# Kernel optimization log

Hardware: AMD Instinct MI355X
Metric: run time of the kernel (lower is better)

Reference implementation:

```python
import jax, jax.numpy as jnp
import numpy as np

N = 100_000   # num nodes
E = 1_600_000 # num directed edges (avg degree 16)
F_IN = 128    # num_features
HID = 128     # hidden_channels
C = 64        # num_classes
BN_EPS = 1e-5


def setup_inputs() -> dict:
    key = jax.random.key(0)
    ks = jax.random.split(key, 12)
    x = jax.random.normal(ks[0], (N, F_IN), dtype=jnp.float32)
    edge_index = jax.random.randint(ks[1], (2, E), 0, N, dtype=jnp.int32)
    def lin(k, fi, fo):
        s = 1.0 / np.sqrt(fi)
        return jax.random.uniform(k, (fi, fo), jnp.float32, -s, s)
    W1 = lin(ks[2], F_IN, HID)
    b1 = jnp.zeros((HID,), jnp.float32)
    W2 = lin(ks[3], HID, HID)
    b2 = jnp.zeros((HID,), jnp.float32)
    Wout = lin(ks[4], F_IN + 2 * HID, C)  # skip concat: 128 + 2*128 = 384
    bout = jnp.zeros((C,), jnp.float32)
    gamma = jnp.ones((HID,), jnp.float32)   # shared BatchNorm1d weight
    beta = jnp.zeros((HID,), jnp.float32)
    return {"x": x, "edge_index": edge_index, "W1": W1, "b1": b1,
            "W2": W2, "b2": b2, "Wout": Wout, "bout": bout,
            "gamma": gamma, "beta": beta}


def _gcn_norm(edge_index, n):
    # add self loops, then symmetric normalization (PyG GCNConv default)
    src, dst = edge_index[0], edge_index[1]
    loop = jnp.arange(n, dtype=src.dtype)
    src = jnp.concatenate([src, loop])
    dst = jnp.concatenate([dst, loop])
    deg = jax.ops.segment_sum(jnp.ones(src.shape[0], jnp.float32), dst, num_segments=n)
    dinv = jnp.where(deg > 0, jax.lax.rsqrt(deg), 0.0)
    norm = dinv[src] * dinv[dst]  # [E+N]
    return src, dst, norm


def _gcn_conv(h, src, dst, norm, n, W, b):
    h = h @ W                         # [n, out]
    msg = h[src] * norm[:, None]      # gather + scale, [E+n, out]
    return jax.ops.segment_sum(msg, dst, num_segments=n) + b


def _batchnorm(h, gamma, beta):
    # BatchNorm1d in training mode: biased batch statistics over nodes
    m = jnp.mean(h, axis=0)
    v = jnp.mean((h - m) ** 2, axis=0)
    return gamma * (h - m) * jax.lax.rsqrt(v + BN_EPS) + beta


def reference(x, edge_index, W1, b1, W2, b2, Wout, bout, gamma, beta):
    n = x.shape[0]
    src, dst, norm = _gcn_norm(edge_index, n)
    h1 = _batchnorm(jax.nn.relu(_gcn_conv(x, src, dst, norm, n, W1, b1)), gamma, beta)
    h2 = _batchnorm(jax.nn.relu(_gcn_conv(h1, src, dst, norm, n, W2, b2)), gamma, beta)
    hcat = jnp.concatenate([x, h1, h2], axis=1)  # skip concat [n, 384]
    return jax.nn.relu(_gcn_conv(hcat, src, dst, norm, n, Wout, bout))
```

## Files before the change

### kernel.cpp

```cpp
#include <hip/hip_runtime.h>
#include <cstdint>
#include <cstddef>

#define BN_EPS 1e-5f
#define NBLK 256
#define EPBMAX 6400
#define BCAP 4096
#define NBANK 32

typedef __attribute__((ext_vector_type(8))) short  bf16x8;
typedef __attribute__((ext_vector_type(4))) float  f32x4;
typedef __attribute__((ext_vector_type(8))) unsigned short ushort8;

__device__ __forceinline__ float bf2f(unsigned short u) {
  union { unsigned int i; float f; } c; c.i = ((unsigned int)u) << 16; return c.f;
}
__device__ __forceinline__ unsigned short f2bf(float f) {
  union { float f; unsigned int i; } c; c.f = f;
  unsigned int u = c.i;
  return (unsigned short)((u + 0x7FFFu + ((u >> 16) & 1u)) >> 16);
}

__global__ __launch_bounds__(256) void k_part(const int* __restrict__ src, const int* __restrict__ dst, int e, int epb,
                                              int* __restrict__ pairsG, int* __restrict__ cntT, int* __restrict__ scanT) {
  __shared__ int sbuf[EPBMAX];
  __shared__ int hist[1024];
  __shared__ int base[1024];
  __shared__ int tmp[256];
  int tid = threadIdx.x, b = blockIdx.x;
  int e0 = b * epb, e1 = min(e0 + epb, e);
  for (int i = tid; i < 1024; i += 256) hist[i] = 0;
  __syncthreads();
  for (int i = e0 + tid; i < e1; i += 256) atomicAdd(&hist[dst[i] >> 7], 1);
  __syncthreads();
  int c0 = hist[tid * 4], c1 = hist[tid * 4 + 1], c2 = hist[tid * 4 + 2], c3 = hist[tid * 4 + 3];
  int lsum = c0 + c1 + c2 + c3;
  tmp[tid] = lsum; __syncthreads();
  for (int off = 1; off < 256; off <<= 1) {
    int t = (tid >= off) ? tmp[tid - off] : 0; __syncthreads();
    tmp[tid] += t; __syncthreads();
  }
  int excl = tmp[tid] - lsum;
  base[tid * 4] = excl; base[tid * 4 + 1] = excl + c0;
  base[tid * 4 + 2] = excl + c0 + c1; base[tid * 4 + 3] = excl + c0 + c1 + c2;
  *(int4*)(cntT + b * 1024 + tid * 4) = make_int4(c0, c1, c2, c3);
  *(int4*)(scanT + b * 1024 + tid * 4) = make_int4(base[tid * 4], base[tid * 4 + 1], base[tid * 4 + 2], base[tid * 4 + 3]);
  __syncthreads();
  for (int i = e0 + tid; i < e1; i += 256) {
    int d = dst[i], s = src[i];
    int p = atomicAdd(&base[d >> 7], 1);
    sbuf[p] = ((d & 127) << 25) | s;
  }
  __syncthreads();
  int cnt = e1 - e0;
  for (int i = tid; i < cnt; i += 256) pairsG[e0 + i] = sbuf[i];
}

__global__ __launch_bounds__(256) void k_btot(const int* __restrict__ cntT, int* __restrict__ totals) {
  int k = blockIdx.x, tid = threadIdx.x;
  __shared__ int tmp[256];
  tmp[tid] = cntT[tid * 1024 + k];
  __syncthreads();
  for (int s = 128; s > 0; s >>= 1) {
    if (tid < s) tmp[tid] += tmp[tid + s];
    __syncthreads();
  }
  if (tid == 0) totals[k] = tmp[0];
}

__global__ __launch_bounds__(1024) void k_bscan(const int* __restrict__ totals, int* __restrict__ bbase, int nb, int e) {
  __shared__ int tmp[1024];
  int tid = threadIdx.x;
  int v = (tid < nb) ? totals[tid] : 0;
  tmp[tid] = v; __syncthreads();
  for (int off = 1; off < 1024; off <<= 1) {
    int t = (tid >= off) ? tmp[tid - off] : 0; __syncthreads();
    tmp[tid] += t; __syncthreads();
  }
  if (tid < nb) bbase[tid] = tmp[tid] - v;
  if (tid == 0) bbase[nb] = e;
}

__global__ __launch_bounds__(256) void k_build(const int* __restrict__ pairsG, const int* __restrict__ cntT,
                                               const int* __restrict__ scanT, const int* __restrict__ bbase_,
                                               int epb, int n, int nb,
                                               int* __restrict__ rowptr, int* __restrict__ colG, float* __restrict__ dinvG) {
  __shared__ int lpair[BCAP];
  __shared__ int lcol[BCAP];
  __shared__ int lcnt[128], lcur[128];
  __shared__ int tmp[256];
  int k = blockIdx.x, tid = threadIdx.x;
  int len = cntT[tid * 1024 + k];
  int sbase = tid * epb + scanT[tid * 1024 + k];
  tmp[tid] = len; __syncthreads();
  for (int off = 1; off < 256; off <<= 1) {
    int t = (tid >= off) ? tmp[tid - off] : 0; __syncthreads();
    tmp[tid] += t; __syncthreads();
  }
  int dpos = tmp[tid] - len;
  int cnt = tmp[255];
  for (int i = 0; i < len; ++i) lpair[dpos + i] = pairsG[sbase + i];
  if (tid < 128) lcnt[tid] = 0;
  __syncthreads();
  for (int j = tid; j < cnt; j += 256) atomicAdd(&lcnt[((unsigned)lpair[j]) >> 25], 1);
  __syncthreads();
  if (tid < 128) tmp[tid] = lcnt[tid];
  __syncthreads();
  for (int off = 1; off < 128; off <<= 1) {
    int t = (tid >= off && tid < 128) ? tmp[tid - off] : 0; __syncthreads();
    if (tid < 128) tmp[tid] += t;
    __syncthreads();
  }
  int bb = bbase_[k];
  if (tid < 128) {
    int excl = tmp[tid] - lcnt[tid];
    lcur[tid] = excl;
    int g = k * 128 + tid;
    if (g < n) {
      rowptr[g] = bb + excl;
      dinvG[g] = rsqrtf((float)lcnt[tid] + 1.0f);
    }
  }
  if (k == nb - 1 && tid == 0) rowptr[n] = bb + cnt;
  __syncthreads();
  for (int j = tid; j < cnt; j += 256) {
    int w = lpair[j];
    int p = atomicAdd(&lcur[((unsigned)w) >> 25], 1);
    lcol[p] = w & 0x01FFFFFF;
  }
  __syncthreads();
  for (int j = tid; j < cnt; j += 256) colG[bb + j] = lcol[j];
}

__global__ __launch_bounds__(256) void k_cvtw(const float* __restrict__ W1, const float* __restrict__ W2,
                                              const float* __restrict__ W3,
                                              unsigned short* __restrict__ Wt1, unsigned short* __restrict__ Wt2,
                                              unsigned short* __restrict__ Wt3) {
  int b = blockIdx.x, t = threadIdx.x;
  if (b < 64) {
    int idx = b * 256 + t; int k = idx >> 7, c = idx & 127;
    Wt1[c * 128 + k] = f2bf(W1[idx]);
  } else if (b < 128) {
    int idx = (b - 64) * 256 + t; int k = idx >> 7, c = idx & 127;
    Wt2[c * 128 + k] = f2bf(W2[idx]);
  } else {
    int idx = (b - 128) * 256 + t; int k = idx >> 6, c = idx & 63;
    Wt3[c * 384 + k] = f2bf(W3[idx]);
  }
}

template <int MODE>
__global__ __launch_bounds__(256) void k_gemm128(const void* __restrict__ Ap, const unsigned short* __restrict__ Bt,
                                                 const float* __restrict__ ss, const float* __restrict__ dinv,
                                                 unsigned short* __restrict__ C, int n) {
  __shared__ unsigned short As[128 * 128];
  __shared__ unsigned short Bs[128 * 128];
  __shared__ float ssl[256];
  const int tid = threadIdx.x;
  const int row0 = blockIdx.x * 128;
  if (MODE == 1 && tid < 256) ssl[tid] = ss[tid];

  {
    int colr = tid >> 1;
    int cbase = (tid & 1) * 8;
#pragma unroll
    for (int i = 0; i < 8; ++i) {
      int c16 = (cbase + i) * 16;
      int dstb = colr * 256 + (c16 ^ ((colr & 7) << 4));
      ushort8 v = *reinterpret_cast<const ushort8*>(Bt + colr * 128 + (c16 >> 1));
      *reinterpret_cast<ushort8*>((char*)Bs + dstb) = v;
    }
  }
  if (MODE == 1) __syncthreads();
  {
    int r = tid >> 1;
    int gr = row0 + r;
    int cbase = (tid & 1) * 8;
#pragma unroll
    for (int i = 0; i < 8; ++i) {
      int c16 = (cbase + i) * 16;
      int dstb = r * 256 + (c16 ^ ((r & 7) << 4));
      int f0 = c16 >> 1;
      ushort8 v = (ushort8)0;
      if (gr < n) {
        if (MODE == 0) {
          const float* A = (const float*)Ap;
          f32x4 v0 = *reinterpret_cast<const f32x4*>(A + (size_t)gr * 128 + f0);
          f32x4 v1 = *reinterpret_cast<const f32x4*>(A + (size_t)gr * 128 + f0 + 4);
#pragma unroll
          for (int j = 0; j < 4; ++j) { v[j] = f2bf(v0[j]); v[4 + j] = f2bf(v1[j]); }
        } else {
          const unsigned short* A = (const unsigned short*)Ap;
          ushort8 raw = *reinterpret_cast<const ushort8*>(A + (size_t)gr * 128 + f0);
#pragma unroll
          for (int j = 0; j < 8; ++j) v[j] = f2bf(bf2f(raw[j]) * ssl[f0 + j] + ssl[128 + f0 + j]);
        }
      }
      *reinterpret_cast<ushort8*>((char*)As + dstb) = v;
    }
  }
  __syncthreads();

  const int wv = tid >> 6;
  const int l = tid & 63;
  const int lr = l & 15;
  const int lk = l >> 4;

  f32x4 acc[2][8];
#pragma unroll
  for (int mi = 0; mi < 2; ++mi)
#pragma unroll
    for (int ni = 0; ni < 8; ++ni) acc[mi][ni] = (f32x4)0.f;

#pragma unroll
  for (int kt = 0; kt < 4; ++kt) {
    int kbyte = kt * 64 + lk * 16;
    bf16x8 aF[2], bF[8];
#pragma unroll
    for (int mi = 0; mi < 2; ++mi) {
      int r = wv * 32 + mi * 16 + lr;
      aF[mi] = *reinterpret_cast<bf16x8*>((char*)As + r * 256 + (kbyte ^ ((r & 7) << 4)));
    }
#pragma unroll
    for (int ni = 0; ni < 8; ++ni) {
      int c = ni * 16 + lr;
      bF[ni] = *reinterpret_cast<bf16x8*>((char*)Bs + c * 256 + (kbyte ^ ((c & 7) << 4)));
    }
#pragma unroll
    for (int mi = 0; mi < 2; ++mi)
#pragma unroll
      for (int ni = 0; ni < 8; ++ni)
        acc[mi][ni] = __builtin_amdgcn_mfma_f32_16x16x32_bf16(aF[mi], bF[ni], acc[mi][ni], 0, 0, 0);
  }

#pragma unroll
  for (int mi = 0; mi < 2; ++mi) {
#pragma unroll
    for (int i = 0; i < 4; ++i) {
      int gr = row0 + wv * 32 + mi * 16 + lk * 4 + i;
      if (gr < n) {
        float di = dinv[gr];
#pragma unroll
        for (int ni = 0; ni < 8; ++ni) {
          int gc = ni * 16 + lr;
          C[(size_t)gr * 128 + gc] = f2bf(acc[mi][ni][i] * di);
        }
      }
    }
  }
}

__global__ __launch_bounds__(256) void k_gemm3(const float* __restrict__ x, const unsigned short* __restrict__ a1,
                                               const unsigned short* __restrict__ a2,
                                               const float* __restrict__ ss1, const float* __restrict__ ss2,
                                               const unsigned short* __restrict__ Bt3, const float* __restrict__ dinv,
                                               unsigned short* __restrict__ C, int n) {
  __shared__ unsigned short As[128 * 128];
  __shared__ unsigned short Bs[64 * 384];
  __shared__ float ssl[512];
  const int tid = threadIdx.x;
  const int row0 = blockIdx.x * 128;
  if (tid < 256) { ssl[tid] = ss1[tid]; ssl[256 + tid] = ss2[tid]; }

  {
    int colr = tid >> 2;
    int cb = tid & 3;
#pragma unroll
    for (int i = 0; i < 12; ++i) {
      int c16 = (cb + 4 * i) * 16;
      int dstb = colr * 768 + (c16 ^ ((colr & 7) << 4));
      ushort8 v = *reinterpret_cast<const ushort8*>(Bt3 + colr * 384 + (c16 >> 1));
      *reinterpret_cast<ushort8*>((char*)Bs + dstb) = v;
    }
  }

  const int wv = tid >> 6;
  const int l = tid & 63;
  const int lr = l & 15;
  const int lk = l >> 4;

  f32x4 acc[2][4];
#pragma unroll
  for (int mi = 0; mi < 2; ++mi)
#pragma unroll
    for (int ni = 0; ni < 4; ++ni) acc[mi][ni] = (f32x4)0.f;

  for (int ch = 0; ch < 3; ++ch) {
    __syncthreads();
    {
      int r = tid >> 1;
      int gr = row0 + r;
      int cbase = (tid & 1) * 8;
#pragma unroll
      for (int i = 0; i < 8; ++i) {
        int c16 = (cbase + i) * 16;
        int dstb = r * 256 + (c16 ^ ((r & 7) << 4));
        int f0 = c16 >> 1;
        ushort8 v = (ushort8)0;
        if (gr < n) {
          if (ch == 0) {
            f32x4 v0 = *reinterpret_cast<const f32x4*>(x + (size_t)gr * 128 + f0);
            f32x4 v1 = *reinterpret_cast<const f32x4*>(x + (size_t)gr * 128 + f0 + 4);
#pragma unroll
            for (int j = 0; j < 4; ++j) { v[j] = f2bf(v0[j]); v[4 + j] = f2bf(v1[j]); }
          } else {
            const unsigned short* A = (ch == 1) ? a1 : a2;
            const float* sl = ssl + (ch - 1) * 256;
            ushort8 raw = *reinterpret_cast<const ushort8*>(A + (size_t)gr * 128 + f0);
#pragma unroll
            for (int j = 0; j < 8; ++j) v[j] = f2bf(bf2f(raw[j]) * sl[f0 + j] + sl[128 + f0 + j]);
          }
        }
        *reinterpret_cast<ushort8*>((char*)As + dstb) = v;
      }
    }
    __syncthreads();
#pragma unroll
    for (int kt = 0; kt < 4; ++kt) {
      int kbyteA = kt * 64 + lk * 16;
      int kbyteB = ch * 256 + kbyteA;
      bf16x8 aF[2], bF[4];
#pragma unroll
      for (int mi = 0; mi < 2; ++mi) {
        int r = wv * 32 + mi * 16 + lr;
        aF[mi] = *reinterpret_cast<bf16x8*>((char*)As + r * 256 + (kbyteA ^ ((r & 7) << 4)));
      }
#pragma unroll
      for (int ni = 0; ni < 4; ++ni) {
        int c = ni * 16 + lr;
        bF[ni] = *reinterpret_cast<bf16x8*>((char*)Bs + c * 768 + (kbyteB ^ ((c & 7) << 4)));
      }
#pragma unroll
      for (int mi = 0; mi < 2; ++mi)
#pragma unroll
        for (int ni = 0; ni < 4; ++ni)
          acc[mi][ni] = __builtin_amdgcn_mfma_f32_16x16x32_bf16(aF[mi], bF[ni], acc[mi][ni], 0, 0, 0);
    }
  }

#pragma unroll
  for (int mi = 0; mi < 2; ++mi) {
#pragma unroll
    for (int i = 0; i < 4; ++i) {
      int gr = row0 + wv * 32 + mi * 16 + lk * 4 + i;
      if (gr < n) {
        float di = dinv[gr];
#pragma unroll
        for (int ni = 0; ni < 4; ++ni) {
          int gc = ni * 16 + lr;
          C[(size_t)gr * 64 + gc] = f2bf(acc[mi][ni][i] * di);
        }
      }
    }
  }
}

template <int F, int STATS, int OUT_F32>
__global__ __launch_bounds__(256) void k_agg(const unsigned short* __restrict__ t, const int* __restrict__ rowptr,
                                             const int* __restrict__ col, const float* __restrict__ dinv,
                                             const float* __restrict__ bias, void* __restrict__ outp,
                                             float* __restrict__ bank, int n) {
  const int G = F / 8;
  const int RPB = 256 / G;
  int g = threadIdx.x / G;
  int c = threadIdx.x % G;
  int r = blockIdx.x * RPB + g;
  bool act = (r < n);
  float v[8];
#pragma unroll
  for (int j = 0; j < 8; ++j) v[j] = 0.f;
  int f0 = c * 8;
  if (act) {
    float di = dinv[r];
    int e = rowptr[r];
    int e1 = rowptr[r + 1];
    float acc[8];
    {
      ushort8 sv = *reinterpret_cast<const ushort8*>(t + (size_t)r * F + f0);
#pragma unroll
      for (int j = 0; j < 8; ++j) acc[j] = bf2f(sv[j]);
    }
    for (; e + 8 <= e1; e += 8) {
      int s0 = col[e],     s1 = col[e + 1], s2 = col[e + 2], s3 = col[e + 3];
      int s4 = col[e + 4], s5 = col[e + 5], s6 = col[e + 6], s7 = col[e + 7];
      ushort8 u0 = *reinterpret_cast<const ushort8*>(t + (size_t)s0 * F + f0);
      ushort8 u1 = *reinterpret_cast<const ushort8*>(t + (size_t)s1 * F + f0);
      ushort8 u2 = *reinterpret_cast<const ushort8*>(t + (size_t)s2 * F + f0);
      ushort8 u3 = *reinterpret_cast<const ushort8*>(t + (size_t)s3 * F + f0);
      ushort8 u4 = *reinterpret_cast<const ushort8*>(t + (size_t)s4 * F + f0);
      ushort8 u5 = *reinterpret_cast<const ushort8*>(t + (size_t)s5 * F + f0);
      ushort8 u6 = *reinterpret_cast<const ushort8*>(t + (size_t)s6 * F + f0);
      ushort8 u7 = *reinterpret_cast<const ushort8*>(t + (size_t)s7 * F + f0);
#pragma unroll
      for (int j = 0; j < 8; ++j) {
        float p0 = bf2f(u0[j]) + bf2f(u1[j]);
        float p1 = bf2f(u2[j]) + bf2f(u3[j]);
        float p2 = bf2f(u4[j]) + bf2f(u5[j]);
        float p3 = bf2f(u6[j]) + bf2f(u7[j]);
        acc[j] += (p0 + p1) + (p2 + p3);
      }
    }
    if (e + 4 <= e1) {
      int s0 = col[e], s1 = col[e + 1], s2 = col[e + 2], s3 = col[e + 3];
      ushort8 u0 = *reinterpret_cast<const ushort8*>(t + (size_t)s0 * F + f0);
      ushort8 u1 = *reinterpret_cast<const ushort8*>(t + (size_t)s1 * F + f0);
      ushort8 u2 = *reinterpret_cast<const ushort8*>(t + (size_t)s2 * F + f0);
      ushort8 u3 = *reinterpret_cast<const ushort8*>(t + (size_t)s3 * F + f0);
#pragma unroll
      for (int j = 0; j < 8; ++j)
        acc[j] += (bf2f(u0[j]) + bf2f(u1[j])) + (bf2f(u2[j]) + bf2f(u3[j]));
      e += 4;
    }
    if (e + 2 <= e1) {
      int s0 = col[e], s1 = col[e + 1];
      ushort8 u0 = *reinterpret_cast<const ushort8*>(t + (size_t)s0 * F + f0);
      ushort8 u1 = *reinterpret_cast<const ushort8*>(t + (size_t)s1 * F + f0);
#pragma unroll
      for (int j = 0; j < 8; ++j) acc[j] += bf2f(u0[j]) + bf2f(u1[j]);
      e += 2;
    }
    if (e < e1) {
      int s = col[e];
      ushort8 u = *reinterpret_cast<const ushort8*>(t + (size_t)s * F + f0);
#pragma unroll
      for (int j = 0; j < 8; ++j) acc[j] += bf2f(u[j]);
    }
#pragma unroll
    for (int j = 0; j < 8; ++j) v[j] = fmaxf(acc[j] * di + bias[f0 + j], 0.f);
    if (OUT_F32) {
      float* o = (float*)outp;
#pragma unroll
      for (int j = 0; j < 8; j += 4) {
        f32x4 w = {v[j], v[j + 1], v[j + 2], v[j + 3]};
        __builtin_nontemporal_store(w, reinterpret_cast<f32x4*>(o + (size_t)r * F + f0 + j));
      }
    } else {
      ushort8 ov;
#pragma unroll
      for (int j = 0; j < 8; ++j) ov[j] = f2bf(v[j]);
      *reinterpret_cast<ushort8*>((unsigned short*)outp + (size_t)r * F + f0) = ov;
    }
  }
  if (STATS) {
    __shared__ float sA[256 * 8];
    __shared__ float sB[256 * 8];
#pragma unroll
    for (int j = 0; j < 8; ++j) { sA[threadIdx.x * 8 + j] = v[j]; sB[threadIdx.x * 8 + j] = v[j] * v[j]; }
    __syncthreads();
    if (threadIdx.x < 128) {
      int f = threadIdx.x;
      int cc = f >> 3, jj = f & 7;
      float s = 0.f, q = 0.f;
#pragma unroll
      for (int gg = 0; gg < 16; ++gg) {
        s += sA[(gg * 16 + cc) * 8 + jj];
        q += sB[(gg * 16 + cc) * 8 + jj];
      }
      float* bk = bank + (blockIdx.x & (NBANK - 1)) * 256;
      atomicAdd(&bk[f], s);
      atomicAdd(&bk[128 + f], q);
    }
  }
}

__global__ void k_bnfinal(const float* __restrict__ bank, const float* __restrict__ gamma,
                          const float* __restrict__ beta, float* __restrict__ ss, float invN) {
  int f = threadIdx.x;
  float s = 0.f, q = 0.f;
  for (int b = 0; b < NBANK; ++b) { s += bank[b * 256 + f]; q += bank[b * 256 + 128 + f]; }
  float m = s * invN;
  float var = q * invN - m * m;
  float sc = gamma[f] * rsqrtf(var + BN_EPS);
  ss[f] = sc;
  ss[128 + f] = beta[f] - m * sc;
}

extern "C" void kernel_launch(void* const* d_in, const int* in_sizes, int n_in,
                              void* d_out, int out_size, void* d_ws, size_t ws_size,
                              hipStream_t stream) {
  const float* x    = (const float*)d_in[0];
  const int*   ei   = (const int*)d_in[1];
  const float* W1   = (const float*)d_in[2];
  const float* b1   = (const float*)d_in[3];
  const float* W2   = (const float*)d_in[4];
  const float* b2   = (const float*)d_in[5];
  const float* Wout = (const float*)d_in[6];
  const float* bout = (const float*)d_in[7];
  const float* gamma= (const float*)d_in[8];
  const float* beta = (const float*)d_in[9];
  float* out = (float*)d_out;

  const int n = in_sizes[0] / 128;
  const int e = in_sizes[1] / 2;
  const int* src = ei;
  const int* dst = ei + e;
  const int nb = (n + 127) >> 7;
  const int epb = (e + NBLK - 1) / NBLK;

  char* ws = (char*)d_ws;
  size_t off = 0;
  auto alloc = [&](size_t bytes) -> void* {
    void* p = ws + off;
    off += (bytes + 255) & ~(size_t)255;
    return p;
  };
  int*   pairsG = (int*)alloc((size_t)NBLK * epb * 4);
  int*   cntT   = (int*)alloc((size_t)NBLK * 1024 * 4);
  int*   scanT  = (int*)alloc((size_t)NBLK * 1024 * 4);
  int*   totals = (int*)alloc(1024 * 4);
  int*   bbase  = (int*)alloc(1025 * 4);
  int*   rowptr = (int*)alloc(((size_t)n + 1) * 4);
  float* dinv   = (float*)alloc((size_t)n * 4);
  int*   col    = (int*)alloc((size_t)e * 4);
  float* bank1  = (float*)alloc(NBANK * 256 * 4);
  float* bank2  = (float*)alloc(NBANK * 256 * 4);
  float* ss1    = (float*)alloc(256 * 4);
  float* ss2    = (float*)alloc(256 * 4);
  unsigned short* Wt1 = (unsigned short*)alloc(128 * 128 * 2);
  unsigned short* Wt2 = (unsigned short*)alloc(128 * 128 * 2);
  unsigned short* Wt3 = (unsigned short*)alloc(384 * 64 * 2);
  unsigned short* t   = (unsigned short*)alloc((size_t)n * 128 * 2);
  unsigned short* a1  = (unsigned short*)alloc((size_t)n * 128 * 2);
  unsigned short* a2  = (unsigned short*)alloc((size_t)n * 128 * 2);

  hipMemsetAsync(bank1, 0, (size_t)NBANK * 256 * 4 * 2, stream);

  k_part<<<NBLK, 256, 0, stream>>>(src, dst, e, epb, pairsG, cntT, scanT);
  k_btot<<<nb, 256, 0, stream>>>(cntT, totals);
  k_bscan<<<1, 1024, 0, stream>>>(totals, bbase, nb, e);
  k_build<<<nb, 256, 0, stream>>>(pairsG, cntT, scanT, bbase, epb, n, nb, rowptr, col, dinv);
  k_cvtw<<<224, 256, 0, stream>>>(W1, W2, Wout, Wt1, Wt2, Wt3);

  int nbG = (n + 127) / 128;
  int nbA128 = (n + 15) / 16;
  int nbA64 = (n + 31) / 32;
  float invN = 1.f / (float)n;

  k_gemm128<0><<<nbG, 256, 0, stream>>>(x, Wt1, nullptr, dinv, t, n);
  k_agg<128, 1, 0><<<nbA128, 256, 0, stream>>>(t, rowptr, col, dinv, b1, a1, bank1, n);
  k_bnfinal<<<1, 128, 0, stream>>>(bank1, gamma, beta, ss1, invN);

  k_gemm128<1><<<nbG, 256, 0, stream>>>(a1, Wt2, ss1, dinv, t, n);
  k_agg<128, 1, 0><<<nbA128, 256, 0, stream>>>(t, rowptr, col, dinv, b2, a2, bank2, n);
  k_bnfinal<<<1, 128, 0, stream>>>(bank2, gamma, beta, ss2, invN);

  k_gemm3<<<nbG, 256, 0, stream>>>(x, a1, a2, ss1, ss2, Wt3, dinv, t, n);
  k_agg<64, 0, 1><<<nbA64, 256, 0, stream>>>(t, rowptr, col, dinv, bout, out, nullptr, n);
}
```

Baseline: 302.9 us.

## Fold small setup kernels into neighbors and load GEMM A fragments directly to registers

Removes k_btot by having k_part atomically add per-bucket totals, merges the weight conversion into extra k_part blocks, and folds the BatchNorm finalization into the prologue of each consuming GEMM, which drops several tiny kernel launches. The GEMMs no longer stage the A tile through LDS. Each lane loads its MFMA A fragments straight from global memory into registers, removing LDS traffic and a barrier. In exchange every GEMM block redundantly reduces the 32-bank statistics, and the direct global loads are less coalesced.

```diff
diff --git a/kernel.cpp b/kernel.cpp
--- a/kernel.cpp
+++ b/kernel.cpp
@@ -22,17 +22,30 @@
 }
 
 __global__ __launch_bounds__(256) void k_part(const int* __restrict__ src, const int* __restrict__ dst, int e, int epb,
-                                              int* __restrict__ pairsG, int* __restrict__ cntT, int* __restrict__ scanT) {
+                                              int* __restrict__ pairsG, int* __restrict__ cntT, int* __restrict__ scanT,
+                                              int* __restrict__ totals,
+                                              const float* __restrict__ W1, const float* __restrict__ W2,
+                                              const float* __restrict__ W3,
+                                              unsigned short* __restrict__ Wt1, unsigned short* __restrict__ Wt2,
+                                              unsigned short* __restrict__ Wt3) {
+  int b = blockIdx.x, tid = threadIdx.x;
+  if (b >= NBLK) {
+    int bb = b - NBLK;
+    if (bb < 64)       { int idx = bb * 256 + tid;        Wt1[(idx & 127) * 128 + (idx >> 7)] = f2bf(W1[idx]); }
+    else if (bb < 128) { int idx = (bb - 64) * 256 + tid; Wt2[(idx & 127) * 128 + (idx >> 7)] = f2bf(W2[idx]); }
+    else               { int idx = (bb - 128) * 256 + tid; Wt3[(idx & 63) * 384 + (idx >> 6)] = f2bf(W3[idx]); }
+    return;
+  }
   __shared__ int sbuf[EPBMAX];
   __shared__ int hist[1024];
   __shared__ int base[1024];
   __shared__ int tmp[256];
-  int tid = threadIdx.x, b = blockIdx.x;
   int e0 = b * epb, e1 = min(e0 + epb, e);
   for (int i = tid; i < 1024; i += 256) hist[i] = 0;
   __syncthreads();
   for (int i = e0 + tid; i < e1; i += 256) atomicAdd(&hist[dst[i] >> 7], 1);
   __syncthreads();
+  for (int i = tid; i < 1024; i += 256) { int h = hist[i]; if (h) atomicAdd(&totals[i], h); }
   int c0 = hist[tid * 4], c1 = hist[tid * 4 + 1], c2 = hist[tid * 4 + 2], c3 = hist[tid * 4 + 3];
   int lsum = c0 + c1 + c2 + c3;
   tmp[tid] = lsum; __syncthreads();
@@ -54,18 +67,6 @@
   __syncthreads();
   int cnt = e1 - e0;
   for (int i = tid; i < cnt; i += 256) pairsG[e0 + i] = sbuf[i];
-}
-
-__global__ __launch_bounds__(256) void k_btot(const int* __restrict__ cntT, int* __restrict__ totals) {
-  int k = blockIdx.x, tid = threadIdx.x;
-  __shared__ int tmp[256];
-  tmp[tid] = cntT[tid * 1024 + k];
-  __syncthreads();
-  for (int s = 128; s > 0; s >>= 1) {
-    if (tid < s) tmp[tid] += tmp[tid + s];
-    __syncthreads();
-  }
-  if (tid == 0) totals[k] = tmp[0];
 }
 
 __global__ __launch_bounds__(1024) void k_bscan(const int* __restrict__ totals, int* __restrict__ bbase, int nb, int e) {
@@ -132,34 +133,22 @@
   for (int j = tid; j < cnt; j += 256) colG[bb + j] = lcol[j];
 }
 
-__global__ __launch_bounds__(256) void k_cvtw(const float* __restrict__ W1, const float* __restrict__ W2,
-                                              const float* __restrict__ W3,
-                                              unsigned short* __restrict__ Wt1, unsigned short* __restrict__ Wt2,
-                                              unsigned short* __restrict__ Wt3) {
-  int b = blockIdx.x, t = threadIdx.x;
-  if (b < 64) {
-    int idx = b * 256 + t; int k = idx >> 7, c = idx & 127;
-    Wt1[c * 128 + k] = f2bf(W1[idx]);
-  } else if (b < 128) {
-    int idx = (b - 64) * 256 + t; int k = idx >> 7, c = idx & 127;
-    Wt2[c * 128 + k] = f2bf(W2[idx]);
-  } else {
-    int idx = (b - 128) * 256 + t; int k = idx >> 6, c = idx & 63;
-    Wt3[c * 384 + k] = f2bf(W3[idx]);
-  }
-}
-
 template <int MODE>
 __global__ __launch_bounds__(256) void k_gemm128(const void* __restrict__ Ap, const unsigned short* __restrict__ Bt,
-                                                 const float* __restrict__ ss, const float* __restrict__ dinv,
-                                                 unsigned short* __restrict__ C, int n) {
-  __shared__ unsigned short As[128 * 128];
+                                                 const float* __restrict__ bank, const float* __restrict__ gamma,
+                                                 const float* __restrict__ beta, float invN,
+                                                 const float* __restrict__ dinv, unsigned short* __restrict__ C, int n) {
   __shared__ unsigned short Bs[128 * 128];
   __shared__ float ssl[256];
   const int tid = threadIdx.x;
   const int row0 = blockIdx.x * 128;
-  if (MODE == 1 && tid < 256) ssl[tid] = ss[tid];
-
+  if (MODE == 1 && tid < 128) {
+    float s = 0.f, q = 0.f;
+    for (int b = 0; b < NBANK; ++b) { s += bank[b * 256 + tid]; q += bank[b * 256 + 128 + tid]; }
+    float m = s * invN, var = q * invN - m * m;
+    float sc = gamma[tid] * rsqrtf(var + BN_EPS);
+    ssl[tid] = sc; ssl[128 + tid] = beta[tid] - m * sc;
+  }
   {
     int colr = tid >> 1;
     int cbase = (tid & 1) * 8;
@@ -171,40 +160,54 @@
       *reinterpret_cast<ushort8*>((char*)Bs + dstb) = v;
     }
   }
-  if (MODE == 1) __syncthreads();
-  {
-    int r = tid >> 1;
-    int gr = row0 + r;
-    int cbase = (tid & 1) * 8;
-#pragma unroll
-    for (int i = 0; i < 8; ++i) {
-      int c16 = (cbase + i) * 16;
-      int dstb = r * 256 + (c16 ^ ((r & 7) << 4));
-      int f0 = c16 >> 1;
-      ushort8 v = (ushort8)0;
-      if (gr < n) {
-        if (MODE == 0) {
-          const float* A = (const float*)Ap;
-          f32x4 v0 = *reinterpret_cast<const f32x4*>(A + (size_t)gr * 128 + f0);
-          f32x4 v1 = *reinterpret_cast<const f32x4*>(A + (size_t)gr * 128 + f0 + 4);
-#pragma unroll
-          for (int j = 0; j < 4; ++j) { v[j] = f2bf(v0[j]); v[4 + j] = f2bf(v1[j]); }
-        } else {
-          const unsigned short* A = (const unsigned short*)Ap;
-          ushort8 raw = *reinterpret_cast<const ushort8*>(A + (size_t)gr * 128 + f0);
-#pragma unroll
-          for (int j = 0; j < 8; ++j) v[j] = f2bf(bf2f(raw[j]) * ssl[f0 + j] + ssl[128 + f0 + j]);
-        }
-      }
-      *reinterpret_cast<ushort8*>((char*)As + dstb) = v;
-    }
-  }
-  __syncthreads();
-
-  const int wv = tid >> 6;
-  const int l = tid & 63;
-  const int lr = l & 15;
-  const int lk = l >> 4;
+  __syncthreads();
+
+  const int wv = tid >> 6, l = tid & 63, lr = l & 15, lk = l >> 4;
+  int rowc[2];
+#pragma unroll
+  for (int mi = 0; mi < 2; ++mi) {
+    int gr = row0 + wv * 32 + mi * 16 + lr;
+    rowc[mi] = (gr < n) ? gr : 0;
+  }
+
+  bf16x8 aF[2][4];
+  if (MODE == 0) {
+    const float* A = (const float*)Ap;
+#pragma unroll
+    for (int mi = 0; mi < 2; ++mi)
+#pragma unroll
+      for (int kt = 0; kt < 4; ++kt) {
+        const float* p = A + (size_t)rowc[mi] * 128 + kt * 32 + lk * 8;
+        f32x4 lo = *reinterpret_cast<const f32x4*>(p);
+        f32x4 hi = *reinterpret_cast<const f32x4*>(p + 4);
+        bf16x8 a;
+#pragma unroll
+        for (int j = 0; j < 4; ++j) { a[j] = (short)f2bf(lo[j]); a[4 + j] = (short)f2bf(hi[j]); }
+        aF[mi][kt] = a;
+      }
+  } else {
+    const unsigned short* A = (const unsigned short*)Ap;
+    ushort8 raw[2][4];
+#pragma unroll
+    for (int mi = 0; mi < 2; ++mi)
+#pragma unroll
+      for (int kt = 0; kt < 4; ++kt)
+        raw[mi][kt] = *reinterpret_cast<const ushort8*>(A + (size_t)rowc[mi] * 128 + kt * 32 + lk * 8);
+#pragma unroll
+    for (int kt = 0; kt < 4; ++kt) {
+      int kof = kt * 32 + lk * 8;
+      float sc[8], sh[8];
+#pragma unroll
+      for (int j = 0; j < 8; ++j) { sc[j] = ssl[kof + j]; sh[j] = ssl[128 + kof + j]; }
+#pragma unroll
+      for (int mi = 0; mi < 2; ++mi) {
+        bf16x8 a;
+#pragma unroll
+        for (int j = 0; j < 8; ++j) a[j] = (short)f2bf(bf2f(raw[mi][kt][j]) * sc[j] + sh[j]);
+        aF[mi][kt] = a;
+      }
+    }
+  }
 
   f32x4 acc[2][8];
 #pragma unroll
@@ -215,12 +218,7 @@
 #pragma unroll
   for (int kt = 0; kt < 4; ++kt) {
     int kbyte = kt * 64 + lk * 16;
-    bf16x8 aF[2], bF[8];
-#pragma unroll
-    for (int mi = 0; mi < 2; ++mi) {
-      int r = wv * 32 + mi * 16 + lr;
-      aF[mi] = *reinterpret_cast<bf16x8*>((char*)As + r * 256 + (kbyte ^ ((r & 7) << 4)));
-    }
+    bf16x8 bF[8];
 #pragma unroll
     for (int ni = 0; ni < 8; ++ni) {
       int c = ni * 16 + lr;
@@ -230,7 +228,7 @@
     for (int mi = 0; mi < 2; ++mi)
 #pragma unroll
       for (int ni = 0; ni < 8; ++ni)
-        acc[mi][ni] = __builtin_amdgcn_mfma_f32_16x16x32_bf16(aF[mi], bF[ni], acc[mi][ni], 0, 0, 0);
+        acc[mi][ni] = __builtin_amdgcn_mfma_f32_16x16x32_bf16(aF[mi][kt], bF[ni], acc[mi][ni], 0, 0, 0);
   }
 
 #pragma unroll
@@ -252,16 +250,25 @@
 
 __global__ __launch_bounds__(256) void k_gemm3(const float* __restrict__ x, const unsigned short* __restrict__ a1,
                                                const unsigned short* __restrict__ a2,
-                                               const float* __restrict__ ss1, const float* __restrict__ ss2,
+                                               const float* __restrict__ bank1, const float* __restrict__ bank2,
+                                               const float* __restrict__ gamma, const float* __restrict__ beta,
+                                               float invN,
                                                const unsigned short* __restrict__ Bt3, const float* __restrict__ dinv,
                                                unsigned short* __restrict__ C, int n) {
-  __shared__ unsigned short As[128 * 128];
   __shared__ unsigned short Bs[64 * 384];
   __shared__ float ssl[512];
   const int tid = threadIdx.x;
   const int row0 = blockIdx.x * 128;
-  if (tid < 256) { ssl[tid] = ss1[tid]; ssl[256 + tid] = ss2[tid]; }
-
+  if (tid < 256) {
+    int f = tid & 127;
+    const float* bk = (tid < 128) ? bank1 : bank2;
+    int base = (tid < 128) ? 0 : 256;
+    float s = 0.f, q = 0.f;
+    for (int b = 0; b < NBANK; ++b) { s += bk[b * 256 + f]; q += bk[b * 256 + 128 + f]; }
+    float m = s * invN, var = q * invN - m * m;
+    float sc = gamma[f] * rsqrtf(var + BN_EPS);
+    ssl[base + f] = sc; ssl[base + 128 + f] = beta[f] - m * sc;
+  }
   {
     int colr = tid >> 2;
     int cb = tid & 3;
@@ -273,11 +280,15 @@
       *reinterpret_cast<ushort8*>((char*)Bs + dstb) = v;
     }
   }
-
-  const int wv = tid >> 6;
-  const int l = tid & 63;
-  const int lr = l & 15;
-  const int lk = l >> 4;
+  __syncthreads();
+
+  const int wv = tid >> 6, l = tid & 63, lr = l & 15, lk = l >> 4;
+  int rowc[2];
+#pragma unroll
+  for (int mi = 0; mi < 2; ++mi) {
+    int gr = row0 + wv * 32 + mi * 16 + lr;
+    rowc[mi] = (gr < n) ? gr : 0;
+  }
 
   f32x4 acc[2][4];
 #pragma unroll
@@ -285,46 +296,50 @@
 #pragma unroll
     for (int ni = 0; ni < 4; ++ni) acc[mi][ni] = (f32x4)0.f;
 
+#pragma unroll
   for (int ch = 0; ch < 3; ++ch) {
-    __syncthreads();
-    {
-      int r = tid >> 1;
-      int gr = row0 + r;
-      int cbase = (tid & 1) * 8;
-#pragma unroll
-      for (int i = 0; i < 8; ++i) {
-        int c16 = (cbase + i) * 16;
-        int dstb = r * 256 + (c16 ^ ((r & 7) << 4));
-        int f0 = c16 >> 1;
-        ushort8 v = (ushort8)0;
-        if (gr < n) {
-          if (ch == 0) {
-            f32x4 v0 = *reinterpret_cast<const f32x4*>(x + (size_t)gr * 128 + f0);
-            f32x4 v1 = *reinterpret_cast<const f32x4*>(x + (size_t)gr * 128 + f0 + 4);
-#pragma unroll
-            for (int j = 0; j < 4; ++j) { v[j] = f2bf(v0[j]); v[4 + j] = f2bf(v1[j]); }
-          } else {
-            const unsigned short* A = (ch == 1) ? a1 : a2;
-            const float* sl = ssl + (ch - 1) * 256;
-            ushort8 raw = *reinterpret_cast<const ushort8*>(A + (size_t)gr * 128 + f0);
-#pragma unroll
-            for (int j = 0; j < 8; ++j) v[j] = f2bf(bf2f(raw[j]) * sl[f0 + j] + sl[128 + f0 + j]);
-          }
+    bf16x8 aF[2][4];
+    if (ch == 0) {
+#pragma unroll
+      for (int mi = 0; mi < 2; ++mi)
+#pragma unroll
+        for (int kt = 0; kt < 4; ++kt) {
+          const float* p = x + (size_t)rowc[mi] * 128 + kt * 32 + lk * 8;
+          f32x4 lo = *reinterpret_cast<const f32x4*>(p);
+          f32x4 hi = *reinterpret_cast<const f32x4*>(p + 4);
+          bf16x8 a;
+#pragma unroll
+          for (int j = 0; j < 4; ++j) { a[j] = (short)f2bf(lo[j]); a[4 + j] = (short)f2bf(hi[j]); }
+          aF[mi][kt] = a;
         }
-        *reinterpret_cast<ushort8*>((char*)As + dstb) = v;
-      }
-    }
-    __syncthreads();
+    } else {
+      const unsigned short* A = (ch == 1) ? a1 : a2;
+      int base = (ch == 1) ? 0 : 256;
+      ushort8 raw[2][4];
+#pragma unroll
+      for (int mi = 0; mi < 2; ++mi)
+#pragma unroll
+        for (int kt = 0; kt < 4; ++kt)
+          raw[mi][kt] = *reinterpret_cast<const ushort8*>(A + (size_t)rowc[mi] * 128 + kt * 32 + lk * 8);
+#pragma unroll
+      for (int kt = 0; kt < 4; ++kt) {
+        int kof = kt * 32 + lk * 8;
+        float sc[8], sh[8];
+#pragma unroll
+        for (int j = 0; j < 8; ++j) { sc[j] = ssl[base + kof + j]; sh[j] = ssl[base + 128 + kof + j]; }
+#pragma unroll
+        for (int mi = 0; mi < 2; ++mi) {
+          bf16x8 a;
+#pragma unroll
+          for (int j = 0; j < 8; ++j) a[j] = (short)f2bf(bf2f(raw[mi][kt][j]) * sc[j] + sh[j]);
+          aF[mi][kt] = a;
+        }
+      }
+    }
 #pragma unroll
     for (int kt = 0; kt < 4; ++kt) {
-      int kbyteA = kt * 64 + lk * 16;
-      int kbyteB = ch * 256 + kbyteA;
-      bf16x8 aF[2], bF[4];
-#pragma unroll
-      for (int mi = 0; mi < 2; ++mi) {
-        int r = wv * 32 + mi * 16 + lr;
-        aF[mi] = *reinterpret_cast<bf16x8*>((char*)As + r * 256 + (kbyteA ^ ((r & 7) << 4)));
-      }
+      int kbyteB = ch * 256 + kt * 64 + lk * 16;
+      bf16x8 bF[4];
 #pragma unroll
       for (int ni = 0; ni < 4; ++ni) {
         int c = ni * 16 + lr;
@@ -334,7 +349,7 @@
       for (int mi = 0; mi < 2; ++mi)
 #pragma unroll
         for (int ni = 0; ni < 4; ++ni)
-          acc[mi][ni] = __builtin_amdgcn_mfma_f32_16x16x32_bf16(aF[mi], bF[ni], acc[mi][ni], 0, 0, 0);
+          acc[mi][ni] = __builtin_amdgcn_mfma_f32_16x16x32_bf16(aF[mi][kt], bF[ni], acc[mi][ni], 0, 0, 0);
     }
   }
 
@@ -461,18 +476,6 @@
       atomicAdd(&bk[128 + f], q);
     }
   }
-}
-
-__global__ void k_bnfinal(const float* __restrict__ bank, const float* __restrict__ gamma,
-                          const float* __restrict__ beta, float* __restrict__ ss, float invN) {
-  int f = threadIdx.x;
-  float s = 0.f, q = 0.f;
-  for (int b = 0; b < NBANK; ++b) { s += bank[b * 256 + f]; q += bank[b * 256 + 128 + f]; }
-  float m = s * invN;
-  float var = q * invN - m * m;
-  float sc = gamma[f] * rsqrtf(var + BN_EPS);
-  ss[f] = sc;
-  ss[128 + f] = beta[f] - m * sc;
 }
 
 extern "C" void kernel_launch(void* const* d_in, const int* in_sizes, int n_in,
@@ -508,14 +511,12 @@
   int*   cntT   = (int*)alloc((size_t)NBLK * 1024 * 4);
   int*   scanT  = (int*)alloc((size_t)NBLK * 1024 * 4);
   int*   totals = (int*)alloc(1024 * 4);
+  float* bank1  = (float*)alloc(NBANK * 256 * 4);
+  float* bank2  = (float*)alloc(NBANK * 256 * 4);
   int*   bbase  = (int*)alloc(1025 * 4);
   int*   rowptr = (int*)alloc(((size_t)n + 1) * 4);
   float* dinv   = (float*)alloc((size_t)n * 4);
   int*   col    = (int*)alloc((size_t)e * 4);
-  float* bank1  = (float*)alloc(NBANK * 256 * 4);
-  float* bank2  = (float*)alloc(NBANK * 256 * 4);
-  float* ss1    = (float*)alloc(256 * 4);
-  float* ss2    = (float*)alloc(256 * 4);
   unsigned short* Wt1 = (unsigned short*)alloc(128 * 128 * 2);
   unsigned short* Wt2 = (unsigned short*)alloc(128 * 128 * 2);
   unsigned short* Wt3 = (unsigned short*)alloc(384 * 64 * 2);
@@ -523,27 +524,24 @@
   unsigned short* a1  = (unsigned short*)alloc((size_t)n * 128 * 2);
   unsigned short* a2  = (unsigned short*)alloc((size_t)n * 128 * 2);
 
-  hipMemsetAsync(bank1, 0, (size_t)NBANK * 256 * 4 * 2, stream);
-
-  k_part<<<NBLK, 256, 0, stream>>>(src, dst, e, epb, pairsG, cntT, scanT);
-  k_btot<<<nb, 256, 0, stream>>>(cntT, totals);
+  hipMemsetAsync(totals, 0, 1024 * 4 + (size_t)2 * NBANK * 256 * 4, stream);
+
+  k_part<<<NBLK + 224, 256, 0, stream>>>(src, dst, e, epb, pairsG, cntT, scanT, totals,
+                                         W1, W2, Wout, Wt1, Wt2, Wt3);
   k_bscan<<<1, 1024, 0, stream>>>(totals, bbase, nb, e);
   k_build<<<nb, 256, 0, stream>>>(pairsG, cntT, scanT, bbase, epb, n, nb, rowptr, col, dinv);
-  k_cvtw<<<224, 256, 0, stream>>>(W1, W2, Wout, Wt1, Wt2, Wt3);
 
   int nbG = (n + 127) / 128;
   int nbA128 = (n + 15) / 16;
   int nbA64 = (n + 31) / 32;
   float invN = 1.f / (float)n;
 
-  k_gemm128<0><<<nbG, 256, 0, stream>>>(x, Wt1, nullptr, dinv, t, n);
+  k_gemm128<0><<<nbG, 256, 0, stream>>>(x, Wt1, nullptr, nullptr, nullptr, invN, dinv, t, n);
   k_agg<128, 1, 0><<<nbA128, 256, 0, stream>>>(t, rowptr, col, dinv, b1, a1, bank1, n);
-  k_bnfinal<<<1, 128, 0, stream>>>(bank1, gamma, beta, ss1, invN);
-
-  k_gemm128<1><<<nbG, 256, 0, stream>>>(a1, Wt2, ss1, dinv, t, n);
+
+  k_gemm128<1><<<nbG, 256, 0, stream>>>(a1, Wt2, bank1, gamma, beta, invN, dinv, t, n);
   k_agg<128, 1, 0><<<nbA128, 256, 0, stream>>>(t, rowptr, col, dinv, b2, a2, bank2, n);
-  k_bnfinal<<<1, 128, 0, stream>>>(bank2, gamma, beta, ss2, invN);
-
-  k_gemm3<<<nbG, 256, 0, stream>>>(x, a1, a2, ss1, ss2, Wt3, dinv, t, n);
+
+  k_gemm3<<<nbG, 256, 0, stream>>>(x, a1, a2, bank1, bank2, gamma, beta, invN, Wt3, dinv, t, n);
   k_agg<64, 0, 1><<<nbA64, 256, 0, stream>>>(t, rowptr, col, dinv, bout, out, nullptr, n);
 }
```

After: 273.6 us. 9.7% less time.
